# Optimization experiments

Measured on AMD Instinct MI355X. Metric: run time of the kernel, lower is better.

## Reference

```python
import jax, jax.numpy as jnp
import numpy as np

HIDDEN = 2048
NH = 32       # num query heads
NKV = 8       # num kv heads
D = 64        # head_dim = hidden // NH
BSX, BSY = 32, 32  # block sizes


def setup_inputs() -> dict:
    key = jax.random.key(0)
    ks = jax.random.split(key, 5)
    B, L = 2, 4096  # L = x_dim * y_dim
    w = lambda k, sh, fan: jax.random.normal(k, sh, jnp.float32) * (fan ** -0.5)
    return {
        "hidden_states": jax.random.normal(ks[0], (B, L, HIDDEN), jnp.float32),
        "Wq": w(ks[1], (HIDDEN, NH * D), HIDDEN),
        "Wk": w(ks[2], (HIDDEN, NKV * D), HIDDEN),
        "Wv": w(ks[3], (HIDDEN, NKV * D), HIDDEN),
        "Wo": w(ks[4], (NH * D, HIDDEN), NH * D),
        "x_dim": 64,
        "y_dim": 64,
    }


def _block_split(x, B, bnx, bny, h):
    # einops: 'b (bnx bsx bny bsy) (h d) -> (b bnx bny) (bsx bsy) h d'
    x = x.reshape(B, bnx, BSX, bny, BSY, h, D)
    x = x.transpose(0, 1, 3, 2, 4, 5, 6)  # b bnx bny bsx bsy h d
    return x.reshape(B * bnx * bny, BSX * BSY, h, D)


def reference(hidden_states, Wq, Wk, Wv, Wo, x_dim, y_dim):
    B, L, _ = hidden_states.shape
    bnx, bny = x_dim // BSX, y_dim // BSY
    q = _block_split(hidden_states @ Wq, B, bnx, bny, NH)   # [nb, T, NH, D]
    k = _block_split(hidden_states @ Wk, B, bnx, bny, NKV)  # [nb, T, NKV, D]
    v = _block_split(hidden_states @ Wv, B, bnx, bny, NKV)
    g = NH // NKV  # GQA groups: query head i attends kv head i // g
    k = jnp.repeat(k, g, axis=2)
    v = jnp.repeat(v, g, axis=2)
    scores = jnp.einsum('nqhd,nkhd->nhqk', q, k) * (D ** -0.5)
    p = jax.nn.softmax(scores, axis=-1)
    o = jnp.einsum('nhqk,nkhd->nqhd', p, v)  # [nb, T, NH, D]
    # Faithful to the torch code: plain reshape (does NOT invert the block rearrange)
    o = o.reshape(B, L, NH * D)
    return o @ Wo
```

## Files before the change

### kernel.cpp

```cpp
#include <hip/hip_runtime.h>

typedef __bf16 bf16_t;
typedef __bf16 bf16x8 __attribute__((ext_vector_type(8)));
typedef __bf16 bf16x4 __attribute__((ext_vector_type(4)));
typedef float f32x4 __attribute__((ext_vector_type(4)));
typedef float f32x16 __attribute__((ext_vector_type(16)));
typedef short s16x4 __attribute__((ext_vector_type(4)));

#define MFMA16(A_, B_, C_) __builtin_amdgcn_mfma_f32_16x16x32_bf16((A_), (B_), (C_), 0, 0, 0)
#define MFMA32(A_, B_, C_) __builtin_amdgcn_mfma_f32_32x32x16_bf16((A_), (B_), (C_), 0, 0, 0)

#define QSC 0.18033688011112042f

__device__ __forceinline__ void gload_lds16(const bf16_t* g, bf16_t* l) {
  __builtin_amdgcn_global_load_lds(
      (const __attribute__((address_space(1))) void*)g,
      (__attribute__((address_space(3))) void*)l, 16, 0, 0);
}

__device__ __forceinline__ unsigned cvt_pk_bf16(float a, float b) {
  unsigned r;
  asm("v_cvt_pk_bf16_f32 %0, %1, %2" : "=v"(r) : "v"(a), "v"(b));
  return r;
}

__device__ __forceinline__ s16x4 tr_b16(const bf16_t* p) {
  s16x4 d;
  unsigned off = (unsigned)(size_t)(const __attribute__((address_space(3))) bf16_t*)p;
  asm volatile("ds_read_b64_tr_b16 %0, %1" : "=v"(d) : "v"(off));
  return d;
}

__device__ __forceinline__ void swap32(unsigned a, unsigned b, int hi,
                                       unsigned& ra, unsigned& rb) {
  unsigned bx = (unsigned)__shfl_xor((int)b, 32);
  unsigned ax = (unsigned)__shfl_xor((int)a, 32);
  ra = hi ? a : bx;
  rb = hi ? ax : b;
}

__global__ __launch_bounds__(256) void k_convert(const float* __restrict__ in,
                                                 bf16_t* __restrict__ out, int n4) {
  int i = blockIdx.x * 256 + threadIdx.x;
  if (i >= n4) return;
  float4 v = ((const float4*)in)[i];
  bf16x4 o;
  o[0] = (__bf16)v.x; o[1] = (__bf16)v.y; o[2] = (__bf16)v.z; o[3] = (__bf16)v.w;
  *(bf16x4*)(out + (size_t)i * 4) = o;
}

__global__ __launch_bounds__(256) void k_transpose(const float* __restrict__ in,
                                                   bf16_t* __restrict__ out, int R, int C) {
  __shared__ float tile[64][65];
  int tx = threadIdx.x & 63;
  int ty = threadIdx.x >> 6;
  int bc = blockIdx.x * 64;
  int br = blockIdx.y * 64;
#pragma unroll
  for (int i = ty; i < 64; i += 4)
    tile[i][tx] = in[(size_t)(br + i) * C + bc + tx];
  __syncthreads();
#pragma unroll
  for (int i = ty; i < 64; i += 4)
    out[(size_t)(bc + i) * R + br + tx] = (bf16_t)tile[tx][i];
}

__device__ __forceinline__ int permrow(int r) {
  int b  = r >> 12;
  int l  = r & 4095;
  int ix = (l >> 11) & 1;
  int sx = (l >> 6) & 31;
  int iy = (l >> 5) & 1;
  int sy = l & 31;
  return (b << 12) + (ix << 11) + (iy << 10) + (sx << 5) + sy;
}

template <int MODE>
__global__ __launch_bounds__(256, 2) void k_gemm(
    const bf16_t* __restrict__ A,
    const bf16_t* __restrict__ B0, const bf16_t* __restrict__ B1,
    const bf16_t* __restrict__ B2,
    bf16_t* __restrict__ Cq, bf16_t* __restrict__ Ck, bf16_t* __restrict__ Cv,
    float* __restrict__ Cf) {
  const int K = 2048;
  int bid = blockIdx.x;
  int tm = bid & 63;
  int tn = bid >> 6;

  const bf16_t* Bp;
  int brow;
  if (MODE == 0) {
    if (tn < 16)      { Bp = B0; brow = tn << 7; }
    else if (tn < 20) { Bp = B1; brow = (tn - 16) << 7; }
    else              { Bp = B2; brow = (tn - 20) << 7; }
  } else {
    Bp = B0; brow = tn << 7;
  }

  __shared__ bf16_t As[128 * 64];
  __shared__ bf16_t Bs[128 * 64];

  int tid = threadIdx.x;
  int lane = tid & 63;
  int w = tid >> 6;
  int wm = w >> 1, wn = w & 1;
  int g16 = lane >> 4, cl = lane & 15;
  int lrow = lane >> 3, lcol = (lane & 7) << 3;

  const bf16_t* ag = A + (size_t)(tm * 128 + w * 32 + lrow) * K + lcol;
  const bf16_t* bg = Bp + (size_t)(brow + w * 32 + lrow) * K + lcol;
  bf16_t* al = As + (w * 32) * 64;
  bf16_t* bl = Bs + (w * 32) * 64;

  f32x4 acc[4][4];
#pragma unroll
  for (int i = 0; i < 4; ++i)
#pragma unroll
    for (int j = 0; j < 4; ++j) acc[i][j] = (f32x4)(0.0f);

  for (int kt = 0; kt < K / 64; ++kt) {
#pragma unroll
    for (int i = 0; i < 4; ++i) {
      gload_lds16(ag + (size_t)i * 8 * K + kt * 64, al + i * 8 * 64);
      gload_lds16(bg + (size_t)i * 8 * K + kt * 64, bl + i * 8 * 64);
    }
    __syncthreads();

    bf16x8 af[4][2], bfr[4][2];
#pragma unroll
    for (int mi = 0; mi < 4; ++mi)
#pragma unroll
      for (int kk = 0; kk < 2; ++kk) {
        af[mi][kk]  = *(const bf16x8*)&As[(wm * 64 + mi * 16 + cl) * 64 + kk * 32 + g16 * 8];
        bfr[mi][kk] = *(const bf16x8*)&Bs[(wn * 64 + mi * 16 + cl) * 64 + kk * 32 + g16 * 8];
      }
#pragma unroll
    for (int mi = 0; mi < 4; ++mi)
#pragma unroll
      for (int ni = 0; ni < 4; ++ni)
#pragma unroll
        for (int kk = 0; kk < 2; ++kk)
          acc[mi][ni] = MFMA16(af[mi][kk], bfr[ni][kk], acc[mi][ni]);
    __syncthreads();
  }

#pragma unroll
  for (int mi = 0; mi < 4; ++mi) {
#pragma unroll
    for (int rr = 0; rr < 4; ++rr) {
      int r = tm * 128 + wm * 64 + mi * 16 + g16 * 4 + rr;
      if (MODE == 0) {
        int rp = permrow(r);
#pragma unroll
        for (int ni = 0; ni < 4; ++ni) {
          int c = (tn << 7) + wn * 64 + ni * 16 + cl;
          float v = acc[mi][ni][rr];
          if (c < 2048)      Cq[(size_t)rp * 2048 + c] = (bf16_t)(v * QSC);
          else if (c < 2560) Ck[(size_t)rp * 512 + (c - 2048)] = (bf16_t)v;
          else               Cv[(size_t)rp * 512 + (c - 2560)] = (bf16_t)v;
        }
      } else {
#pragma unroll
        for (int ni = 0; ni < 4; ++ni) {
          int c = (tn << 7) + wn * 64 + ni * 16 + cl;
          Cf[(size_t)r * 2048 + c] = acc[mi][ni][rr];
        }
      }
    }
  }
}

__global__ __launch_bounds__(256, 2) void k_attn(
    const bf16_t* __restrict__ Qp, const bf16_t* __restrict__ Kp,
    const bf16_t* __restrict__ Vp, bf16_t* __restrict__ O) {
  int bid = blockIdx.x;
  int qc = bid & 7;
  int h  = (bid >> 3) & 31;
  int n  = bid >> 8;
  int kvh = h >> 2;

  __shared__ bf16_t buf[2][8192];

  int tid = threadIdx.x, lane = tid & 63, w = tid >> 6;
  int l31 = lane & 31, hi = lane >> 5;
  int qrow_blk = n * 1024 + qc * 128;
  bf16_t* base = &buf[0][0];

#pragma unroll
  for (int r = 0; r < 4; ++r) {
    int ql = r * 32 + (tid >> 3);
    int cs = (tid & 7) << 4;
    int lc = (cs ^ ((ql & 7) << 4)) >> 1;
    gload_lds16(Qp + (size_t)(qrow_blk + ql) * 2048 + h * 64 + lc,
                base + r * 2048 + w * 512);
  }
  __syncthreads();
  bf16x8 qf[4];
  {
    int q = w * 32 + l31;
    const bf16_t* qrow = base + q * 64;
    int sw = (q & 7) << 4;
#pragma unroll
    for (int c = 0; c < 4; ++c)
      qf[c] = *(const bf16x8*)(qrow + (((c * 32 + hi * 16) ^ sw) >> 1));
  }
  __syncthreads();

  f32x16 oacc0 = (f32x16)(0.0f), oacc1 = (f32x16)(0.0f);
  float m_run = -1e30f, l_run = 0.0f;

  auto stageKV = [&](int t) {
    bf16_t* bp = &buf[t & 1][0];
    int kvb = n * 1024 + t * 64;
#pragma unroll
    for (int r = 0; r < 2; ++r) {
      int kv = r * 32 + (tid >> 3);
      int cs = (tid & 7) << 4;
      int lc = (cs ^ ((kv & 7) << 4)) >> 1;
      gload_lds16(Kp + (size_t)(kvb + kv) * 512 + kvh * 64 + lc,
                  bp + r * 2048 + w * 512);
    }
#pragma unroll
    for (int r = 0; r < 2; ++r) {
      int slot = r * 256 + tid;
      int sub = slot >> 3;
      int kb = sub >> 2, db = sub & 3;
      int j = (slot >> 1) & 3, hf = slot & 1;
      gload_lds16(Vp + (size_t)(kvb + kb * 4 + j) * 512 + kvh * 64 + db * 16 + hf * 8,
                  bp + 4096 + r * 2048 + w * 512);
    }
  };

  stageKV(0);
  for (int t = 0; t < 16; ++t) {
    __syncthreads();
    if (t < 15) stageKV(t + 1);
    const bf16_t* bp = &buf[t & 1][0];
    const bf16_t* Vs = bp + 4096;

#pragma unroll
    for (int s = 0; s < 2; ++s) {
      f32x16 st = (f32x16)(0.0f);
      {
        int kv = s * 32 + l31;
        const bf16_t* krow = bp + kv * 64;
        int sw = (kv & 7) << 4;
#pragma unroll
        for (int c = 0; c < 4; ++c) {
          bf16x8 kf = *(const bf16x8*)(krow + (((c * 32 + hi * 16) ^ sw) >> 1));
          st = MFMA32(kf, qf[c], st);
        }
      }
      float a0 = fmaxf(st[0], st[1]),   a1 = fmaxf(st[2], st[3]);
      float a2 = fmaxf(st[4], st[5]),   a3 = fmaxf(st[6], st[7]);
      float a4 = fmaxf(st[8], st[9]),   a5 = fmaxf(st[10], st[11]);
      float a6 = fmaxf(st[12], st[13]), a7 = fmaxf(st[14], st[15]);
      float pmax = fmaxf(fmaxf(fmaxf(a0, a1), fmaxf(a2, a3)),
                         fmaxf(fmaxf(a4, a5), fmaxf(a6, a7)));
      pmax = fmaxf(pmax, __shfl_xor(pmax, 32));
      if (!__all(pmax <= m_run + 11.0f)) {
        float mnew = fmaxf(m_run, pmax);
        float resc = exp2f(m_run - mnew);
        l_run *= resc;
#pragma unroll
        for (int e = 0; e < 16; ++e) { oacc0[e] *= resc; oacc1[e] *= resc; }
        m_run = mnew;
      }
      float rs = 0.0f;
      unsigned pw[8];
#pragma unroll
      for (int u = 0; u < 8; ++u) {
        float p0 = exp2f(st[2 * u] - m_run);
        float p1 = exp2f(st[2 * u + 1] - m_run);
        rs += p0 + p1;
        pw[u] = cvt_pk_bf16(p0, p1);
      }
      rs += __shfl_xor(rs, 32);
      l_run += rs;

#pragma unroll
      for (int c = 0; c < 2; ++c) {
        unsigned w2, w0, w3, w1;
        swap32(pw[c * 4 + 2], pw[c * 4 + 0], hi, w2, w0);
        swap32(pw[c * 4 + 3], pw[c * 4 + 1], hi, w3, w1);
        union { unsigned u[4]; bf16x8 v; } pa;
        pa.u[0] = w0; pa.u[1] = w1; pa.u[2] = w2; pa.u[3] = w3;
        int kb0 = s * 8 + c * 4 + hi * 2;
        int dbl = l31 >> 4;
        int cc8 = (l31 & 15) * 4;
        const bf16_t* p00 = Vs + (kb0 * 4 + dbl) * 64 + cc8;
        const bf16_t* p01 = Vs + ((kb0 + 1) * 4 + dbl) * 64 + cc8;
        const bf16_t* p10 = Vs + (kb0 * 4 + 2 + dbl) * 64 + cc8;
        const bf16_t* p11 = Vs + ((kb0 + 1) * 4 + 2 + dbl) * 64 + cc8;
        s16x4 t00 = tr_b16(p00), t01 = tr_b16(p01);
        s16x4 t10 = tr_b16(p10), t11 = tr_b16(p11);
        asm volatile("s_waitcnt lgkmcnt(0)" ::: "memory");
        __builtin_amdgcn_sched_barrier(0);
        union { s16x4 s4[2]; bf16x8 v; } vf0, vf1;
        vf0.s4[0] = t00; vf0.s4[1] = t01;
        vf1.s4[0] = t10; vf1.s4[1] = t11;
        oacc0 = MFMA32(pa.v, vf0.v, oacc0);
        oacc1 = MFMA32(pa.v, vf1.v, oacc1);
      }
    }
  }

  float linv = 1.0f / l_run;
#pragma unroll
  for (int r = 0; r < 16; ++r) {
    int qrw = (r & 3) + 8 * (r >> 2) + 4 * hi;
    float li = __shfl(linv, qrw);
    size_t orow = (size_t)(qrow_blk + w * 32 + qrw) * 2048 + h * 64 + l31;
    O[orow]      = (bf16_t)(oacc0[r] * li);
    O[orow + 32] = (bf16_t)(oacc1[r] * li);
  }
}

extern "C" void kernel_launch(void* const* d_in, const int* in_sizes, int n_in,
                              void* d_out, int out_size, void* d_ws, size_t ws_size,
                              hipStream_t stream) {
  const float* X  = (const float*)d_in[0];
  const float* Wq = (const float*)d_in[1];
  const float* Wk = (const float*)d_in[2];
  const float* Wv = (const float*)d_in[3];
  const float* Wo = (const float*)d_in[4];
  float* out = (float*)d_out;

  char* ws = (char*)d_ws;
  const size_t MB = 1024 * 1024;
  bf16_t* Xb  = (bf16_t*)(ws + 0);
  bf16_t* WqT = (bf16_t*)(ws + 32 * MB);
  bf16_t* WkT = (bf16_t*)(ws + 40 * MB);
  bf16_t* WvT = (bf16_t*)(ws + 42 * MB);
  bf16_t* WoT = (bf16_t*)(ws + 44 * MB);
  bf16_t* Qp  = (bf16_t*)(ws + 52 * MB);
  bf16_t* Kp  = (bf16_t*)(ws + 84 * MB);
  bf16_t* Vp  = (bf16_t*)(ws + 92 * MB);
  bf16_t* Ob  = (bf16_t*)(ws + 100 * MB);

  k_convert<<<16384, 256, 0, stream>>>(X, Xb, 4194304);
  k_transpose<<<dim3(32, 32), 256, 0, stream>>>(Wq, WqT, 2048, 2048);
  k_transpose<<<dim3(8, 32), 256, 0, stream>>>(Wk, WkT, 2048, 512);
  k_transpose<<<dim3(8, 32), 256, 0, stream>>>(Wv, WvT, 2048, 512);
  k_transpose<<<dim3(32, 32), 256, 0, stream>>>(Wo, WoT, 2048, 2048);

  k_gemm<0><<<1536, 256, 0, stream>>>(Xb, WqT, WkT, WvT, Qp, Kp, Vp, nullptr);
  k_attn<<<2048, 256, 0, stream>>>(Qp, Kp, Vp, Ob);
  k_gemm<1><<<1024, 256, 0, stream>>>(Ob, WoT, nullptr, nullptr, nullptr, nullptr,
                                      nullptr, out);
}
```

Measured before the change: 367.4 us.

## Replace GEMM with 256x256 8-wave double-buffered pipelined kernel

Both projection GEMMs move from a 128x128 tile, 4-wave kernel with a single LDS buffer to a 256x256 tile, 8-wave kernel. The new kernel uses 128 KB of dynamic LDS, double-buffered in half-tile slots, and interleaves global-to-LDS staging with MFMA phases using explicit waitcnt, barriers and setprio. It also XOR-swizzles the LDS layout to avoid bank conflicts and remaps block IDs to group tiles for L2 locality. The aim is more data reuse per loaded tile and load latency hidden behind compute. In exchange the grid is much smaller (384 and 256 workgroups) and the synchronization is fragile hand scheduling.

After: 354.7 us. 3.5% less time.

```diff
diff --git a/kernel.cpp b/kernel.cpp
--- a/kernel.cpp
+++ b/kernel.cpp
@@ -75,85 +75,141 @@
   return (b << 12) + (ix << 11) + (iy << 10) + (sx << 5) + sy;
 }
 
+#define LSLOT(B_, M_, H_) (lds + (((B_)*4 + (M_)*2 + (H_)) << 13))
+
+#define STAGE_A(BUF, HF, T)                                                     \
+  gload_lds16(aB + (size_t)((HF)*128) * 2048 + (T)*64, LSLOT(BUF, 0, HF) + wofs); \
+  gload_lds16(aB + (size_t)((HF)*128 + 64) * 2048 + (T)*64,                     \
+              LSLOT(BUF, 0, HF) + wofs + 4096);
+
+#define STAGE_B(BUF, HF, T)                                                     \
+  gload_lds16(bB + (size_t)((HF)*128) * 2048 + (T)*64, LSLOT(BUF, 1, HF) + wofs); \
+  gload_lds16(bB + (size_t)((HF)*128 + 64) * 2048 + (T)*64,                     \
+              LSLOT(BUF, 1, HF) + wofs + 4096);
+
+#define LOAD_A(BUF, Q)                                                          \
+  { const bf16_t* Ah = LSLOT(BUF, 0, wm);                                       \
+    int r0 = ((Q)*32 + cl) * 64;                                                \
+    af[0][0] = *(const bf16x8*)&Ah[r0 + ((g16 * 8) ^ swz8)];                    \
+    af[0][1] = *(const bf16x8*)&Ah[r0 + ((32 + g16 * 8) ^ swz8)];               \
+    af[1][0] = *(const bf16x8*)&Ah[r0 + 1024 + ((g16 * 8) ^ swz8)];             \
+    af[1][1] = *(const bf16x8*)&Ah[r0 + 1024 + ((32 + g16 * 8) ^ swz8)]; }
+
+#define LOAD_B(BUF)                                                             \
+  { const bf16_t* Bh = LSLOT(BUF, 1, wn >> 1);                                  \
+    _Pragma("unroll") for (int ni = 0; ni < 4; ++ni) {                          \
+      int br = ((wn & 1) * 64 + ni * 16 + cl) * 64;                             \
+      bfr[ni][0] = *(const bf16x8*)&Bh[br + ((g16 * 8) ^ swz8)];                \
+      bfr[ni][1] = *(const bf16x8*)&Bh[br + ((32 + g16 * 8) ^ swz8)]; } }
+
+#define MFMA_QUAD(Q)                                                            \
+  _Pragma("unroll") for (int kk = 0; kk < 2; ++kk)                              \
+    _Pragma("unroll") for (int ni = 0; ni < 4; ++ni) {                          \
+      acc[2*(Q)][ni]   = MFMA16(af[0][kk], bfr[ni][kk], acc[2*(Q)][ni]);        \
+      acc[2*(Q)+1][ni] = MFMA16(af[1][kk], bfr[ni][kk], acc[2*(Q)+1][ni]); }
+
+#define PH_MID(VM4)                                                             \
+  if (VM4) asm volatile("s_waitcnt vmcnt(4)" ::: "memory");                     \
+  __builtin_amdgcn_s_barrier();                                                 \
+  asm volatile("s_waitcnt lgkmcnt(0)" ::: "memory");                            \
+  __builtin_amdgcn_s_setprio(1);
+
+#define PH_END                                                                  \
+  __builtin_amdgcn_s_setprio(0);                                                \
+  __builtin_amdgcn_s_barrier();
+
 template <int MODE>
-__global__ __launch_bounds__(256, 2) void k_gemm(
+__global__ __launch_bounds__(512, 2) void k_gemm8(
     const bf16_t* __restrict__ A,
     const bf16_t* __restrict__ B0, const bf16_t* __restrict__ B1,
     const bf16_t* __restrict__ B2,
     bf16_t* __restrict__ Cq, bf16_t* __restrict__ Ck, bf16_t* __restrict__ Cv,
     float* __restrict__ Cf) {
-  const int K = 2048;
+  extern __shared__ bf16_t lds[];
+
+  int nwg = gridDim.x;
+  int cpx = nwg >> 3;
   int bid = blockIdx.x;
-  int tm = bid & 63;
-  int tn = bid >> 6;
+  int swz = (bid & 7) * cpx + (bid >> 3);
+  int tm = swz & 31;
+  int tn = swz >> 5;
 
   const bf16_t* Bp;
   int brow;
   if (MODE == 0) {
-    if (tn < 16)      { Bp = B0; brow = tn << 7; }
-    else if (tn < 20) { Bp = B1; brow = (tn - 16) << 7; }
-    else              { Bp = B2; brow = (tn - 20) << 7; }
+    if (tn < 8)       { Bp = B0; brow = tn << 8; }
+    else if (tn < 10) { Bp = B1; brow = (tn - 8) << 8; }
+    else              { Bp = B2; brow = (tn - 10) << 8; }
   } else {
-    Bp = B0; brow = tn << 7;
-  }
-
-  __shared__ bf16_t As[128 * 64];
-  __shared__ bf16_t Bs[128 * 64];
+    Bp = B0; brow = tn << 8;
+  }
 
   int tid = threadIdx.x;
   int lane = tid & 63;
   int w = tid >> 6;
-  int wm = w >> 1, wn = w & 1;
+  int wm = w >> 2, wn = w & 3;
   int g16 = lane >> 4, cl = lane & 15;
-  int lrow = lane >> 3, lcol = (lane & 7) << 3;
-
-  const bf16_t* ag = A + (size_t)(tm * 128 + w * 32 + lrow) * K + lcol;
-  const bf16_t* bg = Bp + (size_t)(brow + w * 32 + lrow) * K + lcol;
-  bf16_t* al = As + (w * 32) * 64;
-  bf16_t* bl = Bs + (w * 32) * 64;
-
-  f32x4 acc[4][4];
-#pragma unroll
-  for (int i = 0; i < 4; ++i)
+  int swz8 = (cl & 7) << 3;
+  int wofs = w << 9;
+
+  int srow = tid >> 3;
+  int lc = (((tid & 7) ^ (srow & 7)) << 3);
+  const bf16_t* aB = A + (size_t)(tm * 256 + srow) * 2048 + lc;
+  const bf16_t* bB = Bp + (size_t)(brow + srow) * 2048 + lc;
+
+  f32x4 acc[8][4];
+#pragma unroll
+  for (int i = 0; i < 8; ++i)
 #pragma unroll
     for (int j = 0; j < 4; ++j) acc[i][j] = (f32x4)(0.0f);
 
-  for (int kt = 0; kt < K / 64; ++kt) {
-#pragma unroll
-    for (int i = 0; i < 4; ++i) {
-      gload_lds16(ag + (size_t)i * 8 * K + kt * 64, al + i * 8 * 64);
-      gload_lds16(bg + (size_t)i * 8 * K + kt * 64, bl + i * 8 * 64);
-    }
-    __syncthreads();
-
-    bf16x8 af[4][2], bfr[4][2];
-#pragma unroll
-    for (int mi = 0; mi < 4; ++mi)
-#pragma unroll
-      for (int kk = 0; kk < 2; ++kk) {
-        af[mi][kk]  = *(const bf16x8*)&As[(wm * 64 + mi * 16 + cl) * 64 + kk * 32 + g16 * 8];
-        bfr[mi][kk] = *(const bf16x8*)&Bs[(wn * 64 + mi * 16 + cl) * 64 + kk * 32 + g16 * 8];
-      }
-#pragma unroll
-    for (int mi = 0; mi < 4; ++mi)
-#pragma unroll
-      for (int ni = 0; ni < 4; ++ni)
-#pragma unroll
-        for (int kk = 0; kk < 2; ++kk)
-          acc[mi][ni] = MFMA16(af[mi][kk], bfr[ni][kk], acc[mi][ni]);
-    __syncthreads();
-  }
-
-#pragma unroll
-  for (int mi = 0; mi < 4; ++mi) {
+  STAGE_A(0, 0, 0); STAGE_A(0, 1, 0);
+  STAGE_B(0, 0, 0); STAGE_B(0, 1, 0);
+  STAGE_B(1, 0, 1); STAGE_B(1, 1, 1);
+  asm volatile("s_waitcnt vmcnt(4)" ::: "memory");
+  __builtin_amdgcn_s_barrier();
+
+  for (int it2 = 0; it2 < 16; ++it2) {
+    int t1 = 2 * it2 + 1;
+    int tf = 2 * it2 + 2; if (tf > 31) tf = 31;
+    int tg = 2 * it2 + 3; if (tg > 31) tg = 31;
+    bf16x8 af[2][2], bfr[4][2];
+    LOAD_B(0); LOAD_A(0, 0);
+    STAGE_A(1, 0, t1);
+    PH_MID(0); MFMA_QUAD(0); PH_END;
+    LOAD_A(0, 1);
+    STAGE_A(1, 1, t1);
+    PH_MID(0); MFMA_QUAD(1); PH_END;
+    LOAD_A(0, 2);
+    STAGE_B(0, 0, tf);
+    PH_MID(0); MFMA_QUAD(2); PH_END;
+    LOAD_A(0, 3);
+    STAGE_B(0, 1, tf);
+    PH_MID(1); MFMA_QUAD(3); PH_END;
+    LOAD_B(1); LOAD_A(1, 0);
+    STAGE_A(0, 0, tf);
+    PH_MID(0); MFMA_QUAD(0); PH_END;
+    LOAD_A(1, 1);
+    STAGE_A(0, 1, tf);
+    PH_MID(0); MFMA_QUAD(1); PH_END;
+    LOAD_A(1, 2);
+    STAGE_B(1, 0, tg);
+    PH_MID(0); MFMA_QUAD(2); PH_END;
+    LOAD_A(1, 3);
+    STAGE_B(1, 1, tg);
+    PH_MID(1); MFMA_QUAD(3); PH_END;
+  }
+
+#pragma unroll
+  for (int mi = 0; mi < 8; ++mi) {
 #pragma unroll
     for (int rr = 0; rr < 4; ++rr) {
-      int r = tm * 128 + wm * 64 + mi * 16 + g16 * 4 + rr;
+      int r = tm * 256 + wm * 128 + mi * 16 + g16 * 4 + rr;
       if (MODE == 0) {
         int rp = permrow(r);
 #pragma unroll
         for (int ni = 0; ni < 4; ++ni) {
-          int c = (tn << 7) + wn * 64 + ni * 16 + cl;
+          int c = tn * 256 + wn * 64 + ni * 16 + cl;
           float v = acc[mi][ni][rr];
           if (c < 2048)      Cq[(size_t)rp * 2048 + c] = (bf16_t)(v * QSC);
           else if (c < 2560) Ck[(size_t)rp * 512 + (c - 2048)] = (bf16_t)v;
@@ -162,7 +218,7 @@
       } else {
 #pragma unroll
         for (int ni = 0; ni < 4; ++ni) {
-          int c = (tn << 7) + wn * 64 + ni * 16 + cl;
+          int c = tn * 256 + wn * 64 + ni * 16 + cl;
           Cf[(size_t)r * 2048 + c] = acc[mi][ni][rr];
         }
       }
@@ -338,14 +394,19 @@
   bf16_t* Vp  = (bf16_t*)(ws + 92 * MB);
   bf16_t* Ob  = (bf16_t*)(ws + 100 * MB);
 
+  hipFuncSetAttribute(reinterpret_cast<const void*>(&k_gemm8<0>),
+                      hipFuncAttributeMaxDynamicSharedMemorySize, 131072);
+  hipFuncSetAttribute(reinterpret_cast<const void*>(&k_gemm8<1>),
+                      hipFuncAttributeMaxDynamicSharedMemorySize, 131072);
+
   k_convert<<<16384, 256, 0, stream>>>(X, Xb, 4194304);
   k_transpose<<<dim3(32, 32), 256, 0, stream>>>(Wq, WqT, 2048, 2048);
   k_transpose<<<dim3(8, 32), 256, 0, stream>>>(Wk, WkT, 2048, 512);
   k_transpose<<<dim3(8, 32), 256, 0, stream>>>(Wv, WvT, 2048, 512);
   k_transpose<<<dim3(32, 32), 256, 0, stream>>>(Wo, WoT, 2048, 2048);
 
-  k_gemm<0><<<1536, 256, 0, stream>>>(Xb, WqT, WkT, WvT, Qp, Kp, Vp, nullptr);
+  k_gemm8<0><<<384, 512, 131072, stream>>>(Xb, WqT, WkT, WvT, Qp, Kp, Vp, nullptr);
   k_attn<<<2048, 256, 0, stream>>>(Qp, Kp, Vp, Ob);
-  k_gemm<1><<<1024, 256, 0, stream>>>(Ob, WoT, nullptr, nullptr, nullptr, nullptr,
-                                      nullptr, out);
-}
+  k_gemm8<1><<<256, 512, 131072, stream>>>(Ob, WoT, nullptr, nullptr, nullptr,
+                                           nullptr, nullptr, out);
+}
```
